# Kernel optimization log

Measured on AMD Instinct MI355X. Metric: run time of the kernel, lower is better.

## Reference

```python
import jax, jax.numpy as jnp
import numpy as np

N = 1_000_000          # points
C_IN = 10              # decorated point features
C_OUT = 64             # pillar feature channels
S = 30_000             # number of pillars (segments)
EPS = 1e-3             # BatchNorm1d eps


def setup_inputs() -> dict:
    key = jax.random.key(0)
    ks = jax.random.split(key, 8)
    inputs = jax.random.normal(ks[0], (N, C_IN), dtype=jnp.float32)
    # every pillar gets ~N/S points; sorted, all segments non-empty
    unq_inv = jnp.sort(jnp.arange(N, dtype=jnp.int32) % S)
    W_lin = jax.random.normal(ks[1], (C_OUT, C_IN), dtype=jnp.float32) * 0.3
    gamma = 1.0 + 0.1 * jax.random.normal(ks[2], (C_OUT,), dtype=jnp.float32)
    beta = 0.1 * jax.random.normal(ks[3], (C_OUT,), dtype=jnp.float32)
    dw1 = jax.random.normal(ks[4], (C_OUT,), dtype=jnp.float32) * 0.5      # depthwise 1x1 conv (groups=C)
    pw1 = jax.random.normal(ks[5], (C_OUT, C_OUT), dtype=jnp.float32) * 0.1  # pointwise 1x1 conv
    dw2 = jax.random.normal(ks[6], (C_OUT,), dtype=jnp.float32) * 0.5
    pw2 = jax.random.normal(ks[7], (C_OUT, C_OUT), dtype=jnp.float32) * 0.1
    return {"inputs": inputs, "unq_inv": unq_inv, "W_lin": W_lin,
            "gamma": gamma, "beta": beta, "dw1": dw1, "pw1": pw1,
            "dw2": dw2, "pw2": pw2}


def reference(inputs, unq_inv, W_lin, gamma, beta, dw1, pw1, dw2, pw2):
    # Linear (no bias) -> BN (training-mode batch stats) -> ReLU
    x = inputs @ W_lin.T                                   # [N, C]
    mu = jnp.mean(x, axis=0)
    var = jnp.mean(jnp.square(x - mu), axis=0)             # biased var, as torch BN
    x = (x - mu) * jax.lax.rsqrt(var + EPS) * gamma + beta
    x = jax.nn.relu(x)

    # MAFF attention: local branch (depthwise scale -> swish -> 1x1 conv)
    s = x * dw1                                            # groups=C 1x1 conv == per-channel scale
    xl = (s * jax.nn.sigmoid(s)) @ pw1.T                   # [N, C]
    # global branch: avg-pool over points -> depthwise scale -> relu -> 1x1 conv
    g = jnp.mean(x, axis=0)                                # [C]
    xg = pw2 @ jax.nn.relu(dw2 * g)                        # [C]
    wei = jax.nn.sigmoid(xl + xg)                          # broadcast [N,C] + [C]
    xi = x * (1.0 + wei)

    # segment reductions keyed by pillar id (scatter_max + scatter_sum)
    x_max = jax.ops.segment_max(xi, unq_inv, num_segments=S,
                                indices_are_sorted=True)
    x_sum = jax.ops.segment_sum(xi, unq_inv, num_segments=S,
                                indices_are_sorted=True)
    return x_max + x_sum                                   # [S, C]
```

## Files before the change

### kernel.cpp

```cpp
#include <hip/hip_runtime.h>
#include <math.h>

#define N_PTS   1000000
#define CI      10
#define C       64
#define NSEG    30000
#define BN_EPS  1e-3f

#define NBLK_M  2048
#define NBLK_G  2048
#define P1STR   72
#define P1OFF   32768
#define P2OFF   (P1OFF + NBLK_M * P1STR)
#define FROFF   (P2OFF + NBLK_G * 64)


using f32x4 = __attribute__((ext_vector_type(4))) float;
using s16x8 = __attribute__((ext_vector_type(8))) short;

__device__ inline short f2bf(float x) {
    unsigned u = __float_as_uint(x);
    unsigned r = (u + 0x7fffu + ((u >> 16) & 1u)) >> 16;
    return (short)r;
}
__device__ inline unsigned pack_trunc(float lo, float hi) {
    return (__float_as_uint(hi) & 0xffff0000u) | (__float_as_uint(lo) >> 16);
}
__device__ inline float frcp(float x) { return __builtin_amdgcn_rcpf(x); }
__device__ inline void lds_fence() {
    asm volatile("s_waitcnt lgkmcnt(0)" ::: "memory");
}

struct Rows { float2 r0, r1, r2, r3; };
__device__ inline Rows zrows() {
    Rows R; R.r0 = R.r1 = R.r2 = R.r3 = make_float2(0.f, 0.f); return R;
}

__global__ void __launch_bounds__(256) k_moments(const float* __restrict__ inp,
                                                 const int* __restrict__ idx,
                                                 float* __restrict__ ws,
                                                 int* __restrict__ starts) {
    const int tid = threadIdx.x;
    float v[65];
#pragma unroll
    for (int k = 0; k < 65; ++k) v[k] = 0.f;

    const int NPP = N_PTS / 2;
    for (int pp = blockIdx.x * blockDim.x + tid; pp < NPP; pp += gridDim.x * blockDim.x) {
        const float4* base = (const float4*)(inp + (size_t)pp * 20);
        float4 a = base[0], b4 = base[1], c = base[2], d = base[3], e = base[4];
        float r0[CI] = {a.x, a.y, a.z, a.w, b4.x, b4.y, b4.z, b4.w, c.x, c.y};
        float r1[CI] = {c.z, c.w, d.x, d.y, d.z, d.w, e.x, e.y, e.z, e.w};
#pragma unroll
        for (int i = 0; i < CI; ++i) v[i] += r0[i] + r1[i];
        int kk = 10;
#pragma unroll
        for (int i = 0; i < CI; ++i)
#pragma unroll
            for (int j = i; j < CI; ++j) {
                v[kk] = fmaf(r0[i], r0[j], v[kk]);
                v[kk] = fmaf(r1[i], r1[j], v[kk]);
                ++kk;
            }

        const int p0 = 2 * pp;
        int2 iv = *(const int2*)(idx + p0);
        if (p0 == 0) starts[0] = 0;
        else { int prev = idx[p0 - 1]; if (prev != iv.x) starts[iv.x] = p0; }
        if (iv.x != iv.y) starts[iv.y] = p0 + 1;
    }

#pragma unroll
    for (int k = 0; k < 65; ++k) {
#pragma unroll
        for (int off = 32; off >= 1; off >>= 1)
            v[k] += __shfl_xor(v[k], off, 64);
    }
    __shared__ float red[4 * 65];
    const int wv = tid >> 6, ln = tid & 63;
    if (ln == 0) {
#pragma unroll
        for (int k = 0; k < 65; ++k) red[wv * 65 + k] = v[k];
    }
    __syncthreads();
    if (tid < 65)
        ws[P1OFF + blockIdx.x * P1STR + tid] =
            red[tid] + red[65 + tid] + red[130 + tid] + red[195 + tid];
}

__global__ void __launch_bounds__(256) k_red(float* __restrict__ ws) {
    const int k = blockIdx.x;
    float s = 0.f;
    for (int i = threadIdx.x; i < NBLK_M; i += 256)
        s += ws[P1OFF + i * P1STR + k];
    __shared__ float r[256];
    r[threadIdx.x] = s;
    __syncthreads();
#pragma unroll
    for (int off = 128; off > 0; off >>= 1) {
        if (threadIdx.x < off) r[threadIdx.x] += r[threadIdx.x + off];
        __syncthreads();
    }
    if (threadIdx.x == 0) ws[k] = r[0];
}

__global__ void __launch_bounds__(256) k_gstats(const float* __restrict__ inp,
                                                const float* __restrict__ W,
                                                const float* __restrict__ gamma,
                                                const float* __restrict__ beta,
                                                float* __restrict__ ws) {
    const int tid  = threadIdx.x;
    const int wv   = tid >> 6;
    const int lane = tid & 63;
    const int m = lane & 15;
    const int q = lane >> 4;
    const float inv_n = 1.f / (float)N_PTS;

    __shared__ float wp[C * CI];
    __shared__ float bsh[C];

    if (tid < C) {
        const int c = tid;
        float w[CI];
#pragma unroll
        for (int i = 0; i < CI; ++i) w[i] = W[c * CI + i];
        float mu = 0.f;
#pragma unroll
        for (int i = 0; i < CI; ++i) mu = fmaf(w[i], ws[i], mu);
        mu *= inv_n;
        float ex2 = 0.f;
        int kk = 10;
#pragma unroll
        for (int i = 0; i < CI; ++i)
#pragma unroll
            for (int j = i; j < CI; ++j) {
                float mm = ws[kk];
                float t = w[i] * w[j] * mm;
                ex2 += (i == j) ? t : 2.f * t;
                ++kk;
            }
        ex2 *= inv_n;
        float var = ex2 - mu * mu;
        float rstd = rsqrtf(var + BN_EPS);
        float a = rstd * gamma[c];
        bsh[c] = beta[c] - mu * a;
#pragma unroll
        for (int i = 0; i < CI; ++i) wp[c * CI + i] = a * w[i];
    }
    __syncthreads();

    s16x8 wfr[4];
#pragma unroll
    for (int nt = 0; nt < 4; ++nt) {
        s16x8 t;
#pragma unroll
        for (int j = 0; j < 8; ++j) {
            int k = 8 * q + j;
            t[j] = (k < CI) ? f2bf(wp[(nt * 16 + m) * CI + k]) : (short)0;
        }
        wfr[nt] = t;
    }
    float bb[4];
#pragma unroll
    for (int nt = 0; nt < 4; ++nt) bb[nt] = bsh[nt * 16 + m];

    auto loadrows = [&](int pb) -> Rows {
        Rows R = zrows();
        const float* row = inp + (size_t)(pb + m) * CI;
        if (q == 0) {
            R.r0 = *(const float2*)(row);     R.r1 = *(const float2*)(row + 2);
            R.r2 = *(const float2*)(row + 4); R.r3 = *(const float2*)(row + 6);
        } else if (q == 1) {
            R.r0 = *(const float2*)(row + 8);
        }
        return R;
    };
    auto mkfrag = [&](const Rows& L) -> s16x8 {
        union { s16x8 v; unsigned u[4]; } t;
        t.v = s16x8{0, 0, 0, 0, 0, 0, 0, 0};
        if (q < 2) t.u[0] = pack_trunc(L.r0.x, L.r0.y);
        if (q == 0) {
            t.u[1] = pack_trunc(L.r1.x, L.r1.y);
            t.u[2] = pack_trunc(L.r2.x, L.r2.y);
            t.u[3] = pack_trunc(L.r3.x, L.r3.y);
        }
        return t.v;
    };

    const int wid = blockIdx.x * 4 + wv;
    const int STR = NBLK_G * 4;
    const int NB  = N_PTS / 16;

    float sm[4] = {0.f, 0.f, 0.f, 0.f};
    const f32x4 zero = {0.f, 0.f, 0.f, 0.f};

    Rows Pf0 = zrows(), Pf1 = zrows();
    if (wid < NB) Pf0 = loadrows(wid * 16);
    if (wid + STR < NB) Pf1 = loadrows((wid + STR) * 16);
    int j = 0;
    for (int i = wid; i < NB; i += STR, ++j) {
        Rows L = (j & 1) ? Pf1 : Pf0;
        if (i + 2 * STR < NB) {
            if (j & 1) Pf1 = loadrows((i + 2 * STR) * 16);
            else       Pf0 = loadrows((i + 2 * STR) * 16);
        }
        s16x8 t = mkfrag(L);
#pragma unroll
        for (int nt = 0; nt < 4; ++nt) {
            f32x4 xt = __builtin_amdgcn_mfma_f32_16x16x32_bf16(t, wfr[nt], zero, 0, 0, 0);
#pragma unroll
            for (int r = 0; r < 4; ++r)
                sm[nt] += fmaxf(xt[r] + bb[nt], 0.f);
        }
    }

#pragma unroll
    for (int nt = 0; nt < 4; ++nt) {
        sm[nt] += __shfl_xor(sm[nt], 16, 64);
        sm[nt] += __shfl_xor(sm[nt], 32, 64);
    }
    float S = sm[0];
    if (q == 1) S = sm[1];
    if (q == 2) S = sm[2];
    if (q == 3) S = sm[3];

    __shared__ float red[4 * 64];
    red[wv * 64 + lane] = S;
    __syncthreads();
    if (tid < 64)
        ws[P2OFF + blockIdx.x * 64 + tid] =
            red[tid] + red[64 + tid] + red[128 + tid] + red[192 + tid];
}

__global__ void __launch_bounds__(1024) k_prep(const float* __restrict__ W,
                                               const float* __restrict__ gamma,
                                               const float* __restrict__ beta,
                                               const float* __restrict__ dw1,
                                               const float* __restrict__ pw1,
                                               const float* __restrict__ dw2,
                                               const float* __restrict__ pw2,
                                               float* __restrict__ ws) {
    const int tid = threadIdx.x;
    const int c = tid & 63, g = tid >> 6;
    const float inv_n = 1.f / (float)N_PTS;

    __shared__ float R[1024];
    __shared__ float GS[C], WP[C * CI], BSH[C], T[C], XG[C];

    {
        float s = 0.f;
        for (int i = g; i < NBLK_G; i += 16)
            s += ws[P2OFF + i * 64 + c];
        R[tid] = s;
    }
    __syncthreads();
    if (g == 0) {
        float t = 0.f;
#pragma unroll
        for (int gg = 0; gg < 16; ++gg) t += R[gg * 64 + c];
        GS[c] = t;
    }
    __syncthreads();

    if (tid < C) {
        float w[CI];
#pragma unroll
        for (int i = 0; i < CI; ++i) w[i] = W[tid * CI + i];
        float mu = 0.f;
#pragma unroll
        for (int i = 0; i < CI; ++i) mu = fmaf(w[i], ws[i], mu);
        mu *= inv_n;
        float ex2 = 0.f;
        int kk = 10;
#pragma unroll
        for (int i = 0; i < CI; ++i)
#pragma unroll
            for (int j = i; j < CI; ++j) {
                float mm = ws[kk];
                float t = w[i] * w[j] * mm;
                ex2 += (i == j) ? t : 2.f * t;
                ++kk;
            }
        ex2 *= inv_n;
        float var = ex2 - mu * mu;
        float rstd = rsqrtf(var + BN_EPS);
        float a = rstd * gamma[tid];
        BSH[tid] = beta[tid] - mu * a;
#pragma unroll
        for (int i = 0; i < CI; ++i) WP[tid * CI + i] = a * w[i];
        T[tid] = fmaxf(dw2[tid] * (GS[tid] * inv_n), 0.f);
    }
    __syncthreads();

    if (tid < C) {
        float acc = 0.f;
#pragma unroll
        for (int k = 0; k < C; ++k) acc = fmaf(pw2[tid * C + k], T[k], acc);
        XG[tid] = acc;
    }
    __syncthreads();

    if (tid < C) {
        const int lane = tid, m = lane & 15, q = lane >> 4;
        float4* FR = (float4*)(ws + FROFF);
        union { float4 f; s16x8 v; } u;
#pragma unroll
        for (int nt = 0; nt < 4; ++nt) {
            s16x8 tt;
#pragma unroll
            for (int j = 0; j < 8; ++j) {
                int k = 8 * q + j;
                tt[j] = (k < CI) ? f2bf(WP[(nt * 16 + m) * CI + k]) : (short)0;
            }
            u.v = tt; FR[nt * 64 + lane] = u.f;
        }
#pragma unroll
        for (int nt = 0; nt < 4; ++nt)
#pragma unroll
            for (int kc = 0; kc < 2; ++kc) {
                const float* src = pw1 + (nt * 16 + m) * C + kc * 32 + q * 8;
                float4 p0 = *(const float4*)src, p1 = *(const float4*)(src + 4);
                s16x8 tt;
                tt[0] = f2bf(p0.x); tt[1] = f2bf(p0.y); tt[2] = f2bf(p0.z); tt[3] = f2bf(p0.w);
                tt[4] = f2bf(p1.x); tt[5] = f2bf(p1.y); tt[6] = f2bf(p1.z); tt[7] = f2bf(p1.w);
                u.v = tt; FR[(4 + nt * 2 + kc) * 64 + lane] = u.f;
            }
        float4 f;
        f.x = BSH[m]; f.y = BSH[16 + m]; f.z = BSH[32 + m]; f.w = BSH[48 + m];
        FR[12 * 64 + lane] = f;
        f.x = dw1[m]; f.y = dw1[16 + m]; f.z = dw1[32 + m]; f.w = dw1[48 + m];
        FR[13 * 64 + lane] = f;
        f.x = XG[m]; f.y = XG[16 + m]; f.z = XG[32 + m]; f.w = XG[48 + m];
        FR[14 * 64 + lane] = f;
    }
}

#define LD 68
#define SEGW 2
__global__ void __launch_bounds__(128) k_main(const float* __restrict__ inp,
                                              const float* __restrict__ ws,
                                              const int* __restrict__ starts,
                                              float* __restrict__ out) {
    const int tid  = threadIdx.x;
    const int wv   = tid >> 6;
    const int lane = tid & 63;
    const int m = lane & 15;
    const int q = lane >> 4;
    const f32x4 zero = {0.f, 0.f, 0.f, 0.f};

    const float4* FR = (const float4*)(ws + FROFF);
    union { float4 f; s16x8 v; } u;
    s16x8 wfr[4];
#pragma unroll
    for (int nt = 0; nt < 4; ++nt) { u.f = FR[nt * 64 + lane]; wfr[nt] = u.v; }
    s16x8 bfr[4][2];
#pragma unroll
    for (int nt = 0; nt < 4; ++nt)
#pragma unroll
        for (int kc = 0; kc < 2; ++kc) { u.f = FR[(4 + nt * 2 + kc) * 64 + lane]; bfr[nt][kc] = u.v; }
    const float4 bb4  = FR[12 * 64 + lane];
    const float4 d14  = FR[13 * 64 + lane];
    const float4 xg4  = FR[14 * 64 + lane];
    const float bb[4]  = {bb4.x, bb4.y, bb4.z, bb4.w};
    const float d1v[4] = {d14.x, d14.y, d14.z, d14.w};
    const float xgv[4] = {xg4.x, xg4.y, xg4.z, xg4.w};

    __shared__ float sb[2][16 * LD];
    float* my = sb[wv];

    const int w  = blockIdx.x * 2 + wv;
    const int s0 = w * SEGW;

    int st1 = starts[s0 + 1];
    int st2 = (s0 + 2 < NSEG) ? starts[s0 + 2] : N_PTS;
    const int start   = starts[s0];
    const int end_all = st2;

    int cur = s0;
    int end_cur = st1;

    float sm[4]  = {0.f, 0.f, 0.f, 0.f};
    float mxv[4] = {-INFINITY, -INFINITY, -INFINITY, -INFINITY};

    auto flushseg = [&](int s) {
#pragma unroll
        for (int nt = 0; nt < 4; ++nt) {
            sm[nt] += __shfl_xor(sm[nt], 16, 64);
            sm[nt] += __shfl_xor(sm[nt], 32, 64);
            mxv[nt] = fmaxf(mxv[nt], __shfl_xor(mxv[nt], 16, 64));
            mxv[nt] = fmaxf(mxv[nt], __shfl_xor(mxv[nt], 32, 64));
        }
        float S = sm[0], M = mxv[0];
        if (q == 1) { S = sm[1]; M = mxv[1]; }
        if (q == 2) { S = sm[2]; M = mxv[2]; }
        if (q == 3) { S = sm[3]; M = mxv[3]; }
        out[(size_t)s * C + lane] = S + M;
#pragma unroll
        for (int nt = 0; nt < 4; ++nt) { sm[nt] = 0.f; mxv[nt] = -INFINITY; }
    };

    auto loadrows = [&](int pb) -> Rows {
        Rows R = zrows();
        const float* row = inp + (size_t)min(pb + m, N_PTS - 1) * CI;
        if (q == 0) {
            R.r0 = *(const float2*)(row);     R.r1 = *(const float2*)(row + 2);
            R.r2 = *(const float2*)(row + 4); R.r3 = *(const float2*)(row + 6);
        } else if (q == 1) {
            R.r0 = *(const float2*)(row + 8);
        }
        return R;
    };
    auto mkfrag = [&](const Rows& L) -> s16x8 {
        union { s16x8 v; unsigned u[4]; } t;
        t.v = s16x8{0, 0, 0, 0, 0, 0, 0, 0};
        if (q < 2) t.u[0] = pack_trunc(L.r0.x, L.r0.y);
        if (q == 0) {
            t.u[1] = pack_trunc(L.r1.x, L.r1.y);
            t.u[2] = pack_trunc(L.r2.x, L.r2.y);
            t.u[3] = pack_trunc(L.r3.x, L.r3.y);
        }
        return t.v;
    };

    Rows PA = loadrows(start);
    Rows PB = (start + 16 < end_all) ? loadrows(start + 16) : PA;

    for (int base = start; base < end_all; base += 16) {
        Rows L = PA;
        PA = PB;
        if (base + 32 < end_all) PB = loadrows(base + 32);

        const int nb = min(16, end_all - base);

        s16x8 t = mkfrag(L);
        f32x4 xt[4];
#pragma unroll
        for (int nt = 0; nt < 4; ++nt)
            xt[nt] = __builtin_amdgcn_mfma_f32_16x16x32_bf16(t, wfr[nt], zero, 0, 0, 0);

        float xn[4][4];
#pragma unroll
        for (int nt = 0; nt < 4; ++nt)
#pragma unroll
            for (int r = 0; r < 4; ++r) {
                float x = fmaxf(xt[nt][r] + bb[nt], 0.f);
                xn[nt][r] = x;
                float sg = x * d1v[nt];
                float sw = sg * frcp(1.f + __expf(-sg));
                my[(4 * q + r) * LD + nt * 16 + m] = sw;
            }
        lds_fence();

        s16x8 av[2];
#pragma unroll
        for (int kc = 0; kc < 2; ++kc) {
            const float* src = &my[m * LD + kc * 32 + q * 8];
            float4 p0 = *(const float4*)src;
            float4 p1 = *(const float4*)(src + 4);
            union { s16x8 v; unsigned u[4]; } tt;
            tt.u[0] = pack_trunc(p0.x, p0.y);
            tt.u[1] = pack_trunc(p0.z, p0.w);
            tt.u[2] = pack_trunc(p1.x, p1.y);
            tt.u[3] = pack_trunc(p1.z, p1.w);
            av[kc] = tt.v;
        }

        f32x4 xi[4];
#pragma unroll
        for (int nt = 0; nt < 4; ++nt) {
            xi[nt] = __builtin_amdgcn_mfma_f32_16x16x32_bf16(av[0], bfr[nt][0], zero, 0, 0, 0);
            xi[nt] = __builtin_amdgcn_mfma_f32_16x16x32_bf16(av[1], bfr[nt][1], xi[nt], 0, 0, 0);
        }

#pragma unroll
        for (int nt = 0; nt < 4; ++nt)
#pragma unroll
            for (int r = 0; r < 4; ++r) {
                float v   = xi[nt][r] + xgv[nt];
                float wei = frcp(1.f + __expf(-v));
                float x   = xn[nt][r];
                xi[nt][r] = fmaf(x, wei, x);
            }

        const int fin = base + nb;
        if (fin <= end_cur) {
            if (nb == 16) {
#pragma unroll
                for (int nt = 0; nt < 4; ++nt)
#pragma unroll
                    for (int r = 0; r < 4; ++r) {
                        sm[nt] += xi[nt][r];
                        mxv[nt] = fmaxf(mxv[nt], xi[nt][r]);
                    }
            } else {
#pragma unroll
                for (int nt = 0; nt < 4; ++nt)
#pragma unroll
                    for (int r = 0; r < 4; ++r) {
                        bool act = (4 * q + r) < nb;
                        sm[nt] += act ? xi[nt][r] : 0.f;
                        mxv[nt] = fmaxf(mxv[nt], act ? xi[nt][r] : -INFINITY);
                    }
            }
            if (fin == end_cur) { flushseg(cur); ++cur; end_cur = st2; }
        } else {
            const int B = end_cur - base;
#pragma unroll
            for (int nt = 0; nt < 4; ++nt)
#pragma unroll
                for (int r = 0; r < 4; ++r) {
                    bool act = (4 * q + r) < B;
                    sm[nt] += act ? xi[nt][r] : 0.f;
                    mxv[nt] = fmaxf(mxv[nt], act ? xi[nt][r] : -INFINITY);
                }
            flushseg(cur); ++cur;
#pragma unroll
            for (int nt = 0; nt < 4; ++nt)
#pragma unroll
                for (int r = 0; r < 4; ++r) {
                    int pt = 4 * q + r;
                    bool act = (pt >= B) && (pt < nb);
                    sm[nt] += act ? xi[nt][r] : 0.f;
                    mxv[nt] = fmaxf(mxv[nt], act ? xi[nt][r] : -INFINITY);
                }
            end_cur = st2;
        }
    }
}

extern "C" void kernel_launch(void* const* d_in, const int* in_sizes, int n_in,
                              void* d_out, int out_size, void* d_ws, size_t ws_size,
                              hipStream_t stream) {
    const float* inp   = (const float*)d_in[0];
    const int*   unq   = (const int*)d_in[1];
    const float* W     = (const float*)d_in[2];
    const float* gamma = (const float*)d_in[3];
    const float* beta  = (const float*)d_in[4];
    const float* dw1   = (const float*)d_in[5];
    const float* pw1   = (const float*)d_in[6];
    const float* dw2   = (const float*)d_in[7];
    const float* pw2   = (const float*)d_in[8];
    float* out = (float*)d_out;
    float* ws  = (float*)d_ws;
    int* starts = (int*)ws + 1024;

    k_moments <<<NBLK_M, 256, 0, stream>>>(inp, unq, ws, starts);
    k_red     <<<65,     256, 0, stream>>>(ws);
    k_gstats  <<<NBLK_G, 256, 0, stream>>>(inp, W, gamma, beta, ws);
    k_prep    <<<1,     1024, 0, stream>>>(W, gamma, beta, dw1, pw1, dw2, pw2, ws);
    k_main    <<<7500,   128, 0, stream>>>(inp, ws, starts, out);
}
```

Measured before the change: 294.8 us.

## Fold reduction and prep kernels into atomics and a last-block epilogue

Removes the separate k_red and k_prep launches. Partial moments and global-pool sums are now accumulated with atomicAdd into a memset workspace, and the last block of k_gstats, detected with a counter, builds the MFMA fragments. k_gstats and k_main move to one-wave blocks with contiguous chunking and a deeper three-stage prefetch. The sigmoid/swish exponent constants are also pre-scaled by -log2e so exp2f can be used directly. Float atomics make the summation order nondeterministic and add contention on a few addresses.

```diff
diff --git a/kernel.cpp b/kernel.cpp
--- a/kernel.cpp
+++ b/kernel.cpp
@@ -6,13 +6,9 @@
 #define C       64
 #define NSEG    30000
 #define BN_EPS  1e-3f
-
-#define NBLK_M  2048
-#define NBLK_G  2048
-#define P1STR   72
-#define P1OFF   32768
-#define P2OFF   (P1OFF + NBLK_M * P1STR)
-#define FROFF   (P2OFF + NBLK_G * 64)
+#define FROFF   31104
+#define LOG2E   1.44269504f
+#define NBLK_G  8192
 
 
 using f32x4 = __attribute__((ext_vector_type(4))) float;
@@ -84,185 +80,30 @@
     }
     __syncthreads();
     if (tid < 65)
-        ws[P1OFF + blockIdx.x * P1STR + tid] =
-            red[tid] + red[65 + tid] + red[130 + tid] + red[195 + tid];
-}
-
-__global__ void __launch_bounds__(256) k_red(float* __restrict__ ws) {
-    const int k = blockIdx.x;
-    float s = 0.f;
-    for (int i = threadIdx.x; i < NBLK_M; i += 256)
-        s += ws[P1OFF + i * P1STR + k];
-    __shared__ float r[256];
-    r[threadIdx.x] = s;
-    __syncthreads();
-#pragma unroll
-    for (int off = 128; off > 0; off >>= 1) {
-        if (threadIdx.x < off) r[threadIdx.x] += r[threadIdx.x + off];
-        __syncthreads();
-    }
-    if (threadIdx.x == 0) ws[k] = r[0];
-}
-
-__global__ void __launch_bounds__(256) k_gstats(const float* __restrict__ inp,
-                                                const float* __restrict__ W,
-                                                const float* __restrict__ gamma,
-                                                const float* __restrict__ beta,
-                                                float* __restrict__ ws) {
+        atomicAdd(&ws[tid], red[tid] + red[65 + tid] + red[130 + tid] + red[195 + tid]);
+}
+
+__global__ void __launch_bounds__(64, 4) k_gstats(const float* __restrict__ inp,
+                                                  const float* __restrict__ W,
+                                                  const float* __restrict__ gamma,
+                                                  const float* __restrict__ beta,
+                                                  const float* __restrict__ dw1,
+                                                  const float* __restrict__ pw1,
+                                                  const float* __restrict__ dw2,
+                                                  const float* __restrict__ pw2,
+                                                  float* __restrict__ ws) {
     const int tid  = threadIdx.x;
-    const int wv   = tid >> 6;
-    const int lane = tid & 63;
-    const int m = lane & 15;
-    const int q = lane >> 4;
+    const int m = tid & 15;
+    const int q = tid >> 4;
     const float inv_n = 1.f / (float)N_PTS;
-
-    __shared__ float wp[C * CI];
-    __shared__ float bsh[C];
-
-    if (tid < C) {
-        const int c = tid;
-        float w[CI];
-#pragma unroll
-        for (int i = 0; i < CI; ++i) w[i] = W[c * CI + i];
-        float mu = 0.f;
-#pragma unroll
-        for (int i = 0; i < CI; ++i) mu = fmaf(w[i], ws[i], mu);
-        mu *= inv_n;
-        float ex2 = 0.f;
-        int kk = 10;
-#pragma unroll
-        for (int i = 0; i < CI; ++i)
-#pragma unroll
-            for (int j = i; j < CI; ++j) {
-                float mm = ws[kk];
-                float t = w[i] * w[j] * mm;
-                ex2 += (i == j) ? t : 2.f * t;
-                ++kk;
-            }
-        ex2 *= inv_n;
-        float var = ex2 - mu * mu;
-        float rstd = rsqrtf(var + BN_EPS);
-        float a = rstd * gamma[c];
-        bsh[c] = beta[c] - mu * a;
-#pragma unroll
-        for (int i = 0; i < CI; ++i) wp[c * CI + i] = a * w[i];
-    }
-    __syncthreads();
-
-    s16x8 wfr[4];
-#pragma unroll
-    for (int nt = 0; nt < 4; ++nt) {
-        s16x8 t;
-#pragma unroll
-        for (int j = 0; j < 8; ++j) {
-            int k = 8 * q + j;
-            t[j] = (k < CI) ? f2bf(wp[(nt * 16 + m) * CI + k]) : (short)0;
-        }
-        wfr[nt] = t;
-    }
-    float bb[4];
-#pragma unroll
-    for (int nt = 0; nt < 4; ++nt) bb[nt] = bsh[nt * 16 + m];
-
-    auto loadrows = [&](int pb) -> Rows {
-        Rows R = zrows();
-        const float* row = inp + (size_t)(pb + m) * CI;
-        if (q == 0) {
-            R.r0 = *(const float2*)(row);     R.r1 = *(const float2*)(row + 2);
-            R.r2 = *(const float2*)(row + 4); R.r3 = *(const float2*)(row + 6);
-        } else if (q == 1) {
-            R.r0 = *(const float2*)(row + 8);
-        }
-        return R;
-    };
-    auto mkfrag = [&](const Rows& L) -> s16x8 {
-        union { s16x8 v; unsigned u[4]; } t;
-        t.v = s16x8{0, 0, 0, 0, 0, 0, 0, 0};
-        if (q < 2) t.u[0] = pack_trunc(L.r0.x, L.r0.y);
-        if (q == 0) {
-            t.u[1] = pack_trunc(L.r1.x, L.r1.y);
-            t.u[2] = pack_trunc(L.r2.x, L.r2.y);
-            t.u[3] = pack_trunc(L.r3.x, L.r3.y);
-        }
-        return t.v;
-    };
-
-    const int wid = blockIdx.x * 4 + wv;
-    const int STR = NBLK_G * 4;
-    const int NB  = N_PTS / 16;
-
-    float sm[4] = {0.f, 0.f, 0.f, 0.f};
     const f32x4 zero = {0.f, 0.f, 0.f, 0.f};
 
-    Rows Pf0 = zrows(), Pf1 = zrows();
-    if (wid < NB) Pf0 = loadrows(wid * 16);
-    if (wid + STR < NB) Pf1 = loadrows((wid + STR) * 16);
-    int j = 0;
-    for (int i = wid; i < NB; i += STR, ++j) {
-        Rows L = (j & 1) ? Pf1 : Pf0;
-        if (i + 2 * STR < NB) {
-            if (j & 1) Pf1 = loadrows((i + 2 * STR) * 16);
-            else       Pf0 = loadrows((i + 2 * STR) * 16);
-        }
-        s16x8 t = mkfrag(L);
-#pragma unroll
-        for (int nt = 0; nt < 4; ++nt) {
-            f32x4 xt = __builtin_amdgcn_mfma_f32_16x16x32_bf16(t, wfr[nt], zero, 0, 0, 0);
-#pragma unroll
-            for (int r = 0; r < 4; ++r)
-                sm[nt] += fmaxf(xt[r] + bb[nt], 0.f);
-        }
-    }
-
-#pragma unroll
-    for (int nt = 0; nt < 4; ++nt) {
-        sm[nt] += __shfl_xor(sm[nt], 16, 64);
-        sm[nt] += __shfl_xor(sm[nt], 32, 64);
-    }
-    float S = sm[0];
-    if (q == 1) S = sm[1];
-    if (q == 2) S = sm[2];
-    if (q == 3) S = sm[3];
-
-    __shared__ float red[4 * 64];
-    red[wv * 64 + lane] = S;
-    __syncthreads();
-    if (tid < 64)
-        ws[P2OFF + blockIdx.x * 64 + tid] =
-            red[tid] + red[64 + tid] + red[128 + tid] + red[192 + tid];
-}
-
-__global__ void __launch_bounds__(1024) k_prep(const float* __restrict__ W,
-                                               const float* __restrict__ gamma,
-                                               const float* __restrict__ beta,
-                                               const float* __restrict__ dw1,
-                                               const float* __restrict__ pw1,
-                                               const float* __restrict__ dw2,
-                                               const float* __restrict__ pw2,
-                                               float* __restrict__ ws) {
-    const int tid = threadIdx.x;
-    const int c = tid & 63, g = tid >> 6;
-    const float inv_n = 1.f / (float)N_PTS;
-
-    __shared__ float R[1024];
-    __shared__ float GS[C], WP[C * CI], BSH[C], T[C], XG[C];
+    __shared__ float WP[C * CI];
+    __shared__ float BSH[C];
+    __shared__ float T[C];
+    __shared__ int   lastFlag;
 
     {
-        float s = 0.f;
-        for (int i = g; i < NBLK_G; i += 16)
-            s += ws[P2OFF + i * 64 + c];
-        R[tid] = s;
-    }
-    __syncthreads();
-    if (g == 0) {
-        float t = 0.f;
-#pragma unroll
-        for (int gg = 0; gg < 16; ++gg) t += R[gg * 64 + c];
-        GS[c] = t;
-    }
-    __syncthreads();
-
-    if (tid < C) {
         float w[CI];
 #pragma unroll
         for (int i = 0; i < CI; ++i) w[i] = W[tid * CI + i];
@@ -288,120 +129,27 @@
         BSH[tid] = beta[tid] - mu * a;
 #pragma unroll
         for (int i = 0; i < CI; ++i) WP[tid * CI + i] = a * w[i];
-        T[tid] = fmaxf(dw2[tid] * (GS[tid] * inv_n), 0.f);
     }
     __syncthreads();
 
-    if (tid < C) {
-        float acc = 0.f;
-#pragma unroll
-        for (int k = 0; k < C; ++k) acc = fmaf(pw2[tid * C + k], T[k], acc);
-        XG[tid] = acc;
-    }
-    __syncthreads();
-
-    if (tid < C) {
-        const int lane = tid, m = lane & 15, q = lane >> 4;
-        float4* FR = (float4*)(ws + FROFF);
-        union { float4 f; s16x8 v; } u;
-#pragma unroll
-        for (int nt = 0; nt < 4; ++nt) {
-            s16x8 tt;
-#pragma unroll
-            for (int j = 0; j < 8; ++j) {
-                int k = 8 * q + j;
-                tt[j] = (k < CI) ? f2bf(WP[(nt * 16 + m) * CI + k]) : (short)0;
-            }
-            u.v = tt; FR[nt * 64 + lane] = u.f;
-        }
-#pragma unroll
-        for (int nt = 0; nt < 4; ++nt)
-#pragma unroll
-            for (int kc = 0; kc < 2; ++kc) {
-                const float* src = pw1 + (nt * 16 + m) * C + kc * 32 + q * 8;
-                float4 p0 = *(const float4*)src, p1 = *(const float4*)(src + 4);
-                s16x8 tt;
-                tt[0] = f2bf(p0.x); tt[1] = f2bf(p0.y); tt[2] = f2bf(p0.z); tt[3] = f2bf(p0.w);
-                tt[4] = f2bf(p1.x); tt[5] = f2bf(p1.y); tt[6] = f2bf(p1.z); tt[7] = f2bf(p1.w);
-                u.v = tt; FR[(4 + nt * 2 + kc) * 64 + lane] = u.f;
-            }
-        float4 f;
-        f.x = BSH[m]; f.y = BSH[16 + m]; f.z = BSH[32 + m]; f.w = BSH[48 + m];
-        FR[12 * 64 + lane] = f;
-        f.x = dw1[m]; f.y = dw1[16 + m]; f.z = dw1[32 + m]; f.w = dw1[48 + m];
-        FR[13 * 64 + lane] = f;
-        f.x = XG[m]; f.y = XG[16 + m]; f.z = XG[32 + m]; f.w = XG[48 + m];
-        FR[14 * 64 + lane] = f;
-    }
-}
-
-#define LD 68
-#define SEGW 2
-__global__ void __launch_bounds__(128) k_main(const float* __restrict__ inp,
-                                              const float* __restrict__ ws,
-                                              const int* __restrict__ starts,
-                                              float* __restrict__ out) {
-    const int tid  = threadIdx.x;
-    const int wv   = tid >> 6;
-    const int lane = tid & 63;
-    const int m = lane & 15;
-    const int q = lane >> 4;
-    const f32x4 zero = {0.f, 0.f, 0.f, 0.f};
-
-    const float4* FR = (const float4*)(ws + FROFF);
-    union { float4 f; s16x8 v; } u;
     s16x8 wfr[4];
 #pragma unroll
-    for (int nt = 0; nt < 4; ++nt) { u.f = FR[nt * 64 + lane]; wfr[nt] = u.v; }
-    s16x8 bfr[4][2];
-#pragma unroll
-    for (int nt = 0; nt < 4; ++nt)
-#pragma unroll
-        for (int kc = 0; kc < 2; ++kc) { u.f = FR[(4 + nt * 2 + kc) * 64 + lane]; bfr[nt][kc] = u.v; }
-    const float4 bb4  = FR[12 * 64 + lane];
-    const float4 d14  = FR[13 * 64 + lane];
-    const float4 xg4  = FR[14 * 64 + lane];
-    const float bb[4]  = {bb4.x, bb4.y, bb4.z, bb4.w};
-    const float d1v[4] = {d14.x, d14.y, d14.z, d14.w};
-    const float xgv[4] = {xg4.x, xg4.y, xg4.z, xg4.w};
-
-    __shared__ float sb[2][16 * LD];
-    float* my = sb[wv];
-
-    const int w  = blockIdx.x * 2 + wv;
-    const int s0 = w * SEGW;
-
-    int st1 = starts[s0 + 1];
-    int st2 = (s0 + 2 < NSEG) ? starts[s0 + 2] : N_PTS;
-    const int start   = starts[s0];
-    const int end_all = st2;
-
-    int cur = s0;
-    int end_cur = st1;
-
-    float sm[4]  = {0.f, 0.f, 0.f, 0.f};
-    float mxv[4] = {-INFINITY, -INFINITY, -INFINITY, -INFINITY};
-
-    auto flushseg = [&](int s) {
-#pragma unroll
-        for (int nt = 0; nt < 4; ++nt) {
-            sm[nt] += __shfl_xor(sm[nt], 16, 64);
-            sm[nt] += __shfl_xor(sm[nt], 32, 64);
-            mxv[nt] = fmaxf(mxv[nt], __shfl_xor(mxv[nt], 16, 64));
-            mxv[nt] = fmaxf(mxv[nt], __shfl_xor(mxv[nt], 32, 64));
-        }
-        float S = sm[0], M = mxv[0];
-        if (q == 1) { S = sm[1]; M = mxv[1]; }
-        if (q == 2) { S = sm[2]; M = mxv[2]; }
-        if (q == 3) { S = sm[3]; M = mxv[3]; }
-        out[(size_t)s * C + lane] = S + M;
-#pragma unroll
-        for (int nt = 0; nt < 4; ++nt) { sm[nt] = 0.f; mxv[nt] = -INFINITY; }
-    };
+    for (int nt = 0; nt < 4; ++nt) {
+        s16x8 t;
+#pragma unroll
+        for (int j = 0; j < 8; ++j) {
+            int k = 8 * q + j;
+            t[j] = (k < CI) ? f2bf(WP[(nt * 16 + m) * CI + k]) : (short)0;
+        }
+        wfr[nt] = t;
+    }
+    float bb[4];
+#pragma unroll
+    for (int nt = 0; nt < 4; ++nt) bb[nt] = BSH[nt * 16 + m];
 
     auto loadrows = [&](int pb) -> Rows {
         Rows R = zrows();
-        const float* row = inp + (size_t)min(pb + m, N_PTS - 1) * CI;
+        const float* row = inp + (size_t)(pb + m) * CI;
         if (q == 0) {
             R.r0 = *(const float2*)(row);     R.r1 = *(const float2*)(row + 2);
             R.r2 = *(const float2*)(row + 4); R.r3 = *(const float2*)(row + 6);
@@ -422,13 +170,178 @@
         return t.v;
     };
 
+    const long long NB = N_PTS / 16;
+    const int b0 = (int)((long long)blockIdx.x * NB / NBLK_G);
+    const int b1 = (int)((long long)(blockIdx.x + 1) * NB / NBLK_G);
+
+    float sm[4] = {0.f, 0.f, 0.f, 0.f};
+    Rows P0 = zrows(), P1 = zrows(), P2 = zrows();
+    if (b0 < b1)     P0 = loadrows(b0 * 16);
+    if (b0 + 1 < b1) P1 = loadrows((b0 + 1) * 16);
+    if (b0 + 2 < b1) P2 = loadrows((b0 + 2) * 16);
+
+    for (int b = b0; b < b1; ++b) {
+        Rows L = P0; P0 = P1; P1 = P2;
+        if (b + 3 < b1) P2 = loadrows((b + 3) * 16);
+        s16x8 t = mkfrag(L);
+#pragma unroll
+        for (int nt = 0; nt < 4; ++nt) {
+            f32x4 xt = __builtin_amdgcn_mfma_f32_16x16x32_bf16(t, wfr[nt], zero, 0, 0, 0);
+#pragma unroll
+            for (int r = 0; r < 4; ++r)
+                sm[nt] += fmaxf(xt[r] + bb[nt], 0.f);
+        }
+    }
+
+#pragma unroll
+    for (int nt = 0; nt < 4; ++nt) {
+        sm[nt] += __shfl_xor(sm[nt], 16, 64);
+        sm[nt] += __shfl_xor(sm[nt], 32, 64);
+    }
+    float S = sm[0];
+    if (q == 1) S = sm[1];
+    if (q == 2) S = sm[2];
+    if (q == 3) S = sm[3];
+    atomicAdd(&ws[256 + tid], S);
+
+    __threadfence();
+    if (tid == 0) {
+        int old = atomicAdd((int*)&ws[66], 1);
+        lastFlag = (old == (int)gridDim.x - 1);
+    }
+    __syncthreads();
+    if (!lastFlag) return;
+
+    float g = atomicAdd(&ws[256 + tid], 0.f) * inv_n;
+    T[tid] = fmaxf(dw2[tid] * g, 0.f);
+    __syncthreads();
+    float xg = 0.f;
+#pragma unroll
+    for (int k = 0; k < C; ++k) xg = fmaf(pw2[tid * C + k], T[k], xg);
+    T[tid] = xg;
+    __syncthreads();
+
+    float4* FR = (float4*)(ws + FROFF);
+    union { float4 f; s16x8 v; } u;
+#pragma unroll
+    for (int nt = 0; nt < 4; ++nt) { u.v = wfr[nt]; FR[nt * 64 + tid] = u.f; }
+#pragma unroll
+    for (int nt = 0; nt < 4; ++nt)
+#pragma unroll
+        for (int kc = 0; kc < 2; ++kc) {
+            const float* src = pw1 + (nt * 16 + m) * C + kc * 32 + q * 8;
+            float4 p0 = *(const float4*)src, p1 = *(const float4*)(src + 4);
+            s16x8 tt;
+            tt[0] = f2bf(-LOG2E * p0.x); tt[1] = f2bf(-LOG2E * p0.y);
+            tt[2] = f2bf(-LOG2E * p0.z); tt[3] = f2bf(-LOG2E * p0.w);
+            tt[4] = f2bf(-LOG2E * p1.x); tt[5] = f2bf(-LOG2E * p1.y);
+            tt[6] = f2bf(-LOG2E * p1.z); tt[7] = f2bf(-LOG2E * p1.w);
+            u.v = tt; FR[(4 + nt * 2 + kc) * 64 + tid] = u.f;
+        }
+    float4 f;
+    f.x = BSH[m]; f.y = BSH[16 + m]; f.z = BSH[32 + m]; f.w = BSH[48 + m];
+    FR[12 * 64 + tid] = f;
+    f.x = dw1[m]; f.y = dw1[16 + m]; f.z = dw1[32 + m]; f.w = dw1[48 + m];
+    FR[13 * 64 + tid] = f;
+    f.x = -LOG2E * T[m];      f.y = -LOG2E * T[16 + m];
+    f.z = -LOG2E * T[32 + m]; f.w = -LOG2E * T[48 + m];
+    FR[14 * 64 + tid] = f;
+    f.x = -LOG2E * dw1[m];      f.y = -LOG2E * dw1[16 + m];
+    f.z = -LOG2E * dw1[32 + m]; f.w = -LOG2E * dw1[48 + m];
+    FR[15 * 64 + tid] = f;
+}
+
+#define LD 68
+__global__ void __launch_bounds__(64, 4) k_main(const float* __restrict__ inp,
+                                                const float* __restrict__ ws,
+                                                const int* __restrict__ starts,
+                                                float* __restrict__ out) {
+    const int lane = threadIdx.x;
+    const int m = lane & 15;
+    const int q = lane >> 4;
+    const f32x4 zero = {0.f, 0.f, 0.f, 0.f};
+
+    const float4* FR = (const float4*)(ws + FROFF);
+    union { float4 f; s16x8 v; } u;
+    s16x8 wfr[4];
+#pragma unroll
+    for (int nt = 0; nt < 4; ++nt) { u.f = FR[nt * 64 + lane]; wfr[nt] = u.v; }
+    s16x8 bfr[4][2];
+#pragma unroll
+    for (int nt = 0; nt < 4; ++nt)
+#pragma unroll
+        for (int kc = 0; kc < 2; ++kc) { u.f = FR[(4 + nt * 2 + kc) * 64 + lane]; bfr[nt][kc] = u.v; }
+    const float4 bb4  = FR[12 * 64 + lane];
+    const float4 d14  = FR[13 * 64 + lane];
+    const float4 xe4  = FR[14 * 64 + lane];
+    const float4 de4  = FR[15 * 64 + lane];
+    const float bb[4]  = {bb4.x, bb4.y, bb4.z, bb4.w};
+    const float d1v[4] = {d14.x, d14.y, d14.z, d14.w};
+    const float xge[4] = {xe4.x, xe4.y, xe4.z, xe4.w};
+    const float d1e[4] = {de4.x, de4.y, de4.z, de4.w};
+
+    __shared__ float my[16 * LD];
+
+    const int s0 = blockIdx.x * 2;
+    int st1 = starts[s0 + 1];
+    int st2 = (s0 + 2 < NSEG) ? starts[s0 + 2] : N_PTS;
+    const int start   = starts[s0];
+    const int end_all = st2;
+
+    int cur = s0;
+    int end_cur = st1;
+
+    float sm[4]  = {0.f, 0.f, 0.f, 0.f};
+    float mxv[4] = {-INFINITY, -INFINITY, -INFINITY, -INFINITY};
+
+    auto flushseg = [&](int s) {
+#pragma unroll
+        for (int nt = 0; nt < 4; ++nt) {
+            sm[nt] += __shfl_xor(sm[nt], 16, 64);
+            sm[nt] += __shfl_xor(sm[nt], 32, 64);
+            mxv[nt] = fmaxf(mxv[nt], __shfl_xor(mxv[nt], 16, 64));
+            mxv[nt] = fmaxf(mxv[nt], __shfl_xor(mxv[nt], 32, 64));
+        }
+        float S = sm[0], M = mxv[0];
+        if (q == 1) { S = sm[1]; M = mxv[1]; }
+        if (q == 2) { S = sm[2]; M = mxv[2]; }
+        if (q == 3) { S = sm[3]; M = mxv[3]; }
+        out[(size_t)s * C + lane] = S + M;
+#pragma unroll
+        for (int nt = 0; nt < 4; ++nt) { sm[nt] = 0.f; mxv[nt] = -INFINITY; }
+    };
+
+    auto loadrows = [&](int pb) -> Rows {
+        Rows R = zrows();
+        const float* row = inp + (size_t)min(pb + m, N_PTS - 1) * CI;
+        if (q == 0) {
+            R.r0 = *(const float2*)(row);     R.r1 = *(const float2*)(row + 2);
+            R.r2 = *(const float2*)(row + 4); R.r3 = *(const float2*)(row + 6);
+        } else if (q == 1) {
+            R.r0 = *(const float2*)(row + 8);
+        }
+        return R;
+    };
+    auto mkfrag = [&](const Rows& L) -> s16x8 {
+        union { s16x8 v; unsigned u[4]; } t;
+        t.v = s16x8{0, 0, 0, 0, 0, 0, 0, 0};
+        if (q < 2) t.u[0] = pack_trunc(L.r0.x, L.r0.y);
+        if (q == 0) {
+            t.u[1] = pack_trunc(L.r1.x, L.r1.y);
+            t.u[2] = pack_trunc(L.r2.x, L.r2.y);
+            t.u[3] = pack_trunc(L.r3.x, L.r3.y);
+        }
+        return t.v;
+    };
+
     Rows PA = loadrows(start);
     Rows PB = (start + 16 < end_all) ? loadrows(start + 16) : PA;
+    Rows PC = (start + 32 < end_all) ? loadrows(start + 32) : PB;
 
     for (int base = start; base < end_all; base += 16) {
         Rows L = PA;
-        PA = PB;
-        if (base + 32 < end_all) PB = loadrows(base + 32);
+        PA = PB; PB = PC;
+        if (base + 48 < end_all) PC = loadrows(base + 48);
 
         const int nb = min(16, end_all - base);
 
@@ -445,8 +358,8 @@
             for (int r = 0; r < 4; ++r) {
                 float x = fmaxf(xt[nt][r] + bb[nt], 0.f);
                 xn[nt][r] = x;
-                float sg = x * d1v[nt];
-                float sw = sg * frcp(1.f + __expf(-sg));
+                float e  = exp2f(x * d1e[nt]);
+                float sw = x * d1v[nt] * frcp(1.f + e);
                 my[(4 * q + r) * LD + nt * 16 + m] = sw;
             }
         lds_fence();
@@ -476,8 +389,8 @@
         for (int nt = 0; nt < 4; ++nt)
 #pragma unroll
             for (int r = 0; r < 4; ++r) {
-                float v   = xi[nt][r] + xgv[nt];
-                float wei = frcp(1.f + __expf(-v));
+                float e2  = exp2f(xi[nt][r] + xge[nt]);
+                float wei = frcp(1.f + e2);
                 float x   = xn[nt][r];
                 xi[nt][r] = fmaf(x, wei, x);
             }
@@ -544,9 +457,9 @@
     float* ws  = (float*)d_ws;
     int* starts = (int*)ws + 1024;
 
-    k_moments <<<NBLK_M, 256, 0, stream>>>(inp, unq, ws, starts);
-    k_red     <<<65,     256, 0, stream>>>(ws);
-    k_gstats  <<<NBLK_G, 256, 0, stream>>>(inp, W, gamma, beta, ws);
-    k_prep    <<<1,     1024, 0, stream>>>(W, gamma, beta, dw1, pw1, dw2, pw2, ws);
-    k_main    <<<7500,   128, 0, stream>>>(inp, ws, starts, out);
-}
+    hipMemsetAsync(ws, 0, 384 * sizeof(float), stream);
+
+    k_moments <<<2048,  256, 0, stream>>>(inp, unq, ws, starts);
+    k_gstats  <<<NBLK_G, 64, 0, stream>>>(inp, W, gamma, beta, dw1, pw1, dw2, pw2, ws);
+    k_main    <<<15000,  64, 0, stream>>>(inp, ws, starts, out);
+}
```

Result: slower. 518.7 us (+75.9%).
